# Kernel tuning notes

Hardware: AMD Instinct MI355X
Metric: run time of the kernel (lower is better)

Reference implementation:

```python
import jax, jax.numpy as jnp
import numpy as np

EPS = 1e-5  # torch GroupNorm default


def setup_inputs() -> dict:
    key = jax.random.key(0)
    k1, k2, k3 = jax.random.split(key, 3)
    bs, l, dim = 16, 2048, 512
    G, varDim, numCodes = 2, 256, 320
    x = jax.random.normal(k1, (bs, l, dim), dtype=jnp.float32)
    # grouped 1x1 Conv1d weight: (groups, out_per_group, in_per_group)
    proj_w = jax.random.normal(k2, (G, varDim, varDim), dtype=jnp.float32) / np.sqrt(varDim)
    gn_weight = jnp.ones((dim,), dtype=jnp.float32)
    gn_bias = jnp.zeros((dim,), dtype=jnp.float32)
    embeddings = 0.01 * jax.random.normal(k3, (numCodes, 1, varDim), dtype=jnp.float32)
    return {"x": x, "proj_w": proj_w, "gn_weight": gn_weight,
            "gn_bias": gn_bias, "embeddings": embeddings}


def reference(x, proj_w, gn_weight, gn_bias, embeddings):
    bs, l, dim = x.shape
    G, varDim, _ = proj_w.shape
    numCodes = embeddings.shape[0]

    # --- projection: grouped 1x1 conv ---
    xg = x.transpose(0, 2, 1).reshape(bs, G, varDim, l)            # (bs,G,v,l)
    ze_g = jnp.einsum('gov,bgvl->bgol', proj_w, xg)                # (bs,G,v,l)

    # --- Fp32GroupNorm over (C/G * L) per group ---
    zf = ze_g.astype(jnp.float32)
    mean = zf.mean(axis=(2, 3), keepdims=True)
    var = zf.var(axis=(2, 3), keepdims=True)
    zn = (zf - mean) * jax.lax.rsqrt(var + EPS)
    ze = zn.reshape(bs, dim, l) * gn_weight[None, :, None] + gn_bias[None, :, None]
    ze = ze.astype(x.dtype)                                        # (bs,dim,l)

    # --- VQ: nearest code per group (argmin of L2 == argmin of sq dist) ---
    z = ze.reshape(bs, G, varDim, l).transpose(0, 3, 1, 2)         # (bs,l,G,v)
    emb = jnp.broadcast_to(embeddings, (numCodes, G, varDim))      # combineGroups expand
    dots = jnp.einsum('blgv,cgv->blgc', z, emb)                    # (bs,l,G,C)
    e2 = jnp.sum(emb * emb, axis=-1)                               # (C,G)
    dist = e2.T[None, None] - 2.0 * dots                           # ||z||^2 dropped: const over C
    idx = jnp.argmin(dist, axis=-1)                                # (bs,l,G)

    # gather codes per group
    zq = jnp.take_along_axis(
        emb.transpose(1, 0, 2)[None, None],                        # (1,1,G,C,v)
        idx[..., None, None], axis=3).squeeze(3)                   # (bs,l,G,v)
    zq = zq.reshape(bs, l, dim)

    # straight-through estimator; output shape (bs, l, dim)
    ze_bld = ze.transpose(0, 2, 1)
    out = jax.lax.stop_gradient(zq) + ze_bld - jax.lax.stop_gradient(ze_bld)
    return out
```

## Files before the change

kernel.cpp:

```cpp
#include <hip/hip_runtime.h>
#include <math.h>

typedef _Float16 half8_t  __attribute__((ext_vector_type(8)));
typedef _Float16 half4_t  __attribute__((ext_vector_type(4)));
typedef float    floatx16 __attribute__((ext_vector_type(16)));

#define BS   16
#define LL   2048
#define DIMC 512
#define NG   2
#define VD   256
#define NC   320
#define NELEM ((double)(VD*LL))

#define GLL(gsrc, ldst) __builtin_amdgcn_global_load_lds( \
    (const __attribute__((address_space(1))) unsigned int*)(gsrc), \
    (__attribute__((address_space(3))) unsigned int*)(ldst), 16, 0, 0)

__global__ void k_prep(const float* __restrict__ W, const float* __restrict__ emb,
                       _Float16* __restrict__ Wimg, _Float16* __restrict__ Eimg,
                       float* __restrict__ e2f)
{
  const int blk = blockIdx.x, t = threadIdx.x;
  if (blk < 64) {
    int base = (blk * 256 + t) * 8;
    int k = base & 255, c = k >> 5, kk = k & 31;
    int row = (base >> 8) & 255, g = base >> 16;
    float4 v0 = *(const float4*)(W + base);
    float4 v1 = *(const float4*)(W + base + 4);
    float vv[8] = {v0.x, v0.y, v0.z, v0.w, v1.x, v1.y, v1.z, v1.w};
    half8_t hh, ll;
    #pragma unroll
    for (int i = 0; i < 8; ++i) {
      float s = vv[i] * 16.0f;
      _Float16 h = (_Float16)s;
      hh[i] = h; ll[i] = (_Float16)(s - (float)h);
    }
    size_t rb = ((size_t)(g * 8 + c) * 256 + row) * 72;
    *(half8_t*)&Wimg[rb + kk]      = hh;
    *(half8_t*)&Wimg[rb + 32 + kk] = ll;
  } else if (blk < 104) {
    int base = ((blk - 64) * 256 + t) * 8;
    int k = base & 255, c = k >> 5, kk = k & 31;
    int code = base >> 8;
    float4 v0 = *(const float4*)(emb + base);
    float4 v1 = *(const float4*)(emb + base + 4);
    float vv[8] = {v0.x, v0.y, v0.z, v0.w, v1.x, v1.y, v1.z, v1.w};
    half8_t hh, ll;
    #pragma unroll
    for (int i = 0; i < 8; ++i) {
      float s = vv[i] * 64.0f;
      _Float16 h = (_Float16)s;
      hh[i] = h; ll[i] = (_Float16)(s - (float)h);
    }
    size_t rb = ((size_t)c * 320 + code) * 72;
    *(half8_t*)&Eimg[rb + kk]      = hh;
    *(half8_t*)&Eimg[rb + 32 + kk] = ll;
  } else {
    int code = (blk - 104) * 256 + t;
    if (code < NC) {
      const float* er = emb + (size_t)code * VD;
      double s[4] = {0.0, 0.0, 0.0, 0.0};
      for (int v = 0; v < VD; v += 16)
        #pragma unroll
        for (int u = 0; u < 4; ++u) {
          float4 e4 = *(const float4*)(er + v + u * 4);
          s[u] += (double)e4.x * e4.x + (double)e4.y * e4.y
                + (double)e4.z * e4.z + (double)e4.w * e4.w;
        }
      e2f[code] = (float)(64.0 * (s[0] + s[1] + s[2] + s[3]));
    }
  }
}

__global__ __launch_bounds__(256, 2) void k_proj(
    const float* __restrict__ x, const _Float16* __restrict__ Wimg,
    float* __restrict__ ze, double* __restrict__ stats)
{
  __shared__ _Float16 Ah[128][72];
  __shared__ _Float16 Bh[256 * 72];

  const int blk = blockIdx.x;
  const int g  = blk & 1;
  const int m0 = (blk >> 1) * 128;
  const int b  = m0 >> 11;
  const int t  = threadIdx.x;
  const int lane = t & 63, w = t >> 6;
  const int col  = lane & 31, hq = lane >> 5;
  const int mw = (w & 1) * 64, nw = (w >> 1) * 128;

  const char* wbase = (const char*)(Wimg + (size_t)g * 8 * 256 * 72);

  floatx16 acc[2][4];
  #pragma unroll
  for (int i = 0; i < 2; ++i)
    #pragma unroll
    for (int j = 0; j < 4; ++j)
      #pragma unroll
      for (int e = 0; e < 16; ++e) acc[i][j][e] = 0.f;

  for (int c = 0; c < 8; ++c) {
    #pragma unroll
    for (int i = 0; i < 4; ++i) {
      int idx = i * 256 + t;
      int row = idx >> 3, kq = idx & 7;
      float4 v = *(const float4*)(x + ((size_t)(m0 + row)) * DIMC + g * VD + c * 32 + kq * 4);
      half4_t hh, ll;
      { _Float16 h = (_Float16)v.x; hh[0] = h; ll[0] = (_Float16)(v.x - (float)h); }
      { _Float16 h = (_Float16)v.y; hh[1] = h; ll[1] = (_Float16)(v.y - (float)h); }
      { _Float16 h = (_Float16)v.z; hh[2] = h; ll[2] = (_Float16)(v.z - (float)h); }
      { _Float16 h = (_Float16)v.w; hh[3] = h; ll[3] = (_Float16)(v.w - (float)h); }
      *(half4_t*)&Ah[row][kq * 4]      = hh;
      *(half4_t*)&Ah[row][32 + kq * 4] = ll;
    }
    {
      const char* wc = wbase + (size_t)c * 256 * 144;
      #pragma unroll
      for (int i = 0; i < 9; ++i) {
        int off = (w * 9 + i) * 1024 + lane * 16;
        GLL(wc + off, (char*)Bh + off);
      }
    }
    __syncthreads();
    #pragma unroll
    for (int ks = 0; ks < 2; ++ks) {
      const int ko = ks * 16 + hq * 8;
      half8_t azh[2], azl[2], bwh[4], bwl[4];
      #pragma unroll
      for (int i = 0; i < 2; ++i) {
        azh[i] = *(const half8_t*)&Ah[mw + i * 32 + col][ko];
        azl[i] = *(const half8_t*)&Ah[mw + i * 32 + col][32 + ko];
      }
      #pragma unroll
      for (int j = 0; j < 4; ++j) {
        bwh[j] = *(const half8_t*)&Bh[(nw + j * 32 + col) * 72 + ko];
        bwl[j] = *(const half8_t*)&Bh[(nw + j * 32 + col) * 72 + 32 + ko];
      }
      #pragma unroll
      for (int mi = 0; mi < 2; ++mi)
        #pragma unroll
        for (int ni = 0; ni < 4; ++ni) {
          acc[mi][ni] = __builtin_amdgcn_mfma_f32_32x32x16_f16(azh[mi], bwh[ni], acc[mi][ni], 0, 0, 0);
          acc[mi][ni] = __builtin_amdgcn_mfma_f32_32x32x16_f16(azh[mi], bwl[ni], acc[mi][ni], 0, 0, 0);
          acc[mi][ni] = __builtin_amdgcn_mfma_f32_32x32x16_f16(azl[mi], bwh[ni], acc[mi][ni], 0, 0, 0);
        }
    }
    __syncthreads();
  }

  double s1 = 0.0, s2 = 0.0;
  #pragma unroll
  for (int mi = 0; mi < 2; ++mi)
    #pragma unroll
    for (int ni = 0; ni < 4; ++ni)
      #pragma unroll
      for (int r = 0; r < 16; ++r) {
        float vv = acc[mi][ni][r] * 0.0625f;
        double d = (double)vv; s1 += d; s2 += d * d;
        int ml = mw + mi * 32 + (r & 3) + 8 * (r >> 2) + 4 * hq;
        int nl = nw + ni * 32 + col;
        ze[((size_t)(m0 + ml)) * DIMC + g * VD + nl] = vv;
      }
  #pragma unroll
  for (int off = 32; off > 0; off >>= 1) {
    s1 += __shfl_down(s1, off);
    s2 += __shfl_down(s2, off);
  }
  if (lane == 0) {
    atomicAdd(&stats[(b * NG + g) * 2 + 0], s1);
    atomicAdd(&stats[(b * NG + g) * 2 + 1], s2);
  }
}

__global__ __launch_bounds__(256, 2) void k_vq(
    float* __restrict__ zio, const float* __restrict__ emb,
    const _Float16* __restrict__ Eimg,
    const float* __restrict__ gnw, const float* __restrict__ gnb,
    const double* __restrict__ stats, const float* __restrict__ e2f)
{
  __shared__ _Float16 Zs[128][72];
  __shared__ _Float16 Es[320 * 72];
  __shared__ float e2sh[NC];
  __shared__ int idxs[128];

  const int blk = blockIdx.x;
  const int g  = blk & 1;
  const int m0 = (blk >> 1) * 128;
  const int b  = m0 >> 11;
  const int t  = threadIdx.x;
  const int lane = t & 63, w = t >> 6;
  const int col  = lane & 31, hq = lane >> 5;

  const int si = b * NG + g;
  double ss1 = stats[2 * si], ss2 = stats[2 * si + 1];
  double mu = ss1 / NELEM, var = ss2 / NELEM - mu * mu;
  const float mean = (float)mu;
  const float rstd = (float)(1.0 / sqrt(var + 1e-5));

  for (int c = t; c < NC; c += 256) e2sh[c] = e2f[c];

  float* zbase = zio + (size_t)m0 * DIMC + g * VD;
  const float* gw = gnw + g * VD;
  const float* gb = gnb + g * VD;

  floatx16 acc[10];
  #pragma unroll
  for (int i = 0; i < 10; ++i)
    #pragma unroll
    for (int e = 0; e < 16; ++e) acc[i][e] = 0.f;

  for (int c = 0; c < 8; ++c) {
    #pragma unroll
    for (int i = 0; i < 4; ++i) {
      int idx = i * 256 + t;
      int row = idx >> 3, kq = idx & 7;
      float4 v  = *(const float4*)(zbase + (size_t)row * DIMC + c * 32 + kq * 4);
      float4 w4 = *(const float4*)(gw + c * 32 + kq * 4);
      float4 b4 = *(const float4*)(gb + c * 32 + kq * 4);
      float zn0 = (v.x - mean) * rstd * w4.x + b4.x;
      float zn1 = (v.y - mean) * rstd * w4.y + b4.y;
      float zn2 = (v.z - mean) * rstd * w4.z + b4.z;
      float zn3 = (v.w - mean) * rstd * w4.w + b4.w;
      half4_t hh, ll;
      { _Float16 h = (_Float16)zn0; hh[0] = h; ll[0] = (_Float16)(zn0 - (float)h); }
      { _Float16 h = (_Float16)zn1; hh[1] = h; ll[1] = (_Float16)(zn1 - (float)h); }
      { _Float16 h = (_Float16)zn2; hh[2] = h; ll[2] = (_Float16)(zn2 - (float)h); }
      { _Float16 h = (_Float16)zn3; hh[3] = h; ll[3] = (_Float16)(zn3 - (float)h); }
      *(half4_t*)&Zs[row][kq * 4]      = hh;
      *(half4_t*)&Zs[row][32 + kq * 4] = ll;
    }
    {
      const char* ec = (const char*)Eimg + (size_t)c * 320 * 144;
      for (int i = w; i < 45; i += 4) {
        int off = i * 1024 + lane * 16;
        GLL(ec + off, (char*)Es + off);
      }
    }
    __syncthreads();
    #pragma unroll
    for (int ks = 0; ks < 2; ++ks) {
      const int ko = ks * 16 + hq * 8;
      half8_t bzh = *(const half8_t*)&Zs[w * 32 + col][ko];
      half8_t bzl = *(const half8_t*)&Zs[w * 32 + col][32 + ko];
      #pragma unroll
      for (int mt = 0; mt < 10; ++mt) {
        half8_t aeh = *(const half8_t*)&Es[(mt * 32 + col) * 72 + ko];
        half8_t ael = *(const half8_t*)&Es[(mt * 32 + col) * 72 + 32 + ko];
        acc[mt] = __builtin_amdgcn_mfma_f32_32x32x16_f16(aeh, bzh, acc[mt], 0, 0, 0);
        acc[mt] = __builtin_amdgcn_mfma_f32_32x32x16_f16(aeh, bzl, acc[mt], 0, 0, 0);
        acc[mt] = __builtin_amdgcn_mfma_f32_32x32x16_f16(ael, bzh, acc[mt], 0, 0, 0);
      }
    }
    __syncthreads();
  }

  float bv = 3.4e38f; int bi = 0x7fffffff;
  #pragma unroll
  for (int mt = 0; mt < 10; ++mt)
    #pragma unroll
    for (int r = 0; r < 16; ++r) {
      int code = mt * 32 + (r & 3) + 8 * (r >> 2) + 4 * hq;
      float d = e2sh[code] - 2.0f * acc[mt][r];
      if (d < bv || (d == bv && code < bi)) { bv = d; bi = code; }
    }
  {
    float ov = __shfl_xor(bv, 32);
    int   oi = __shfl_xor(bi, 32);
    if (ov < bv || (ov == bv && oi < bi)) { bv = ov; bi = oi; }
  }
  if (hq == 0) idxs[w * 32 + col] = bi;
  __syncthreads();

  #pragma unroll
  for (int it = 0; it < 32; ++it) {
    int idx = it * 256 + t;
    int row = idx >> 6, q4 = (idx & 63) * 4;
    int id = idxs[row];
    float4 e4 = *(const float4*)(emb + (size_t)id * VD + q4);
    *(float4*)(zbase + (size_t)row * DIMC + q4) = e4;
  }
}

extern "C" void kernel_launch(void* const* d_in, const int* in_sizes, int n_in,
                              void* d_out, int out_size, void* d_ws, size_t ws_size,
                              hipStream_t stream) {
  const float* x   = (const float*)d_in[0];
  const float* W   = (const float*)d_in[1];
  const float* gnw = (const float*)d_in[2];
  const float* gnb = (const float*)d_in[3];
  const float* emb = (const float*)d_in[4];
  float* out = (float*)d_out;

  double*   stats = (double*)d_ws;
  float*    e2f   = (float*)((char*)d_ws + 512);
  _Float16* Wimg  = (_Float16*)((char*)d_ws + 2048);
  _Float16* Eimg  = (_Float16*)((char*)d_ws + 591872);

  hipMemsetAsync(d_ws, 0, 512, stream);
  k_prep<<<106, 256, 0, stream>>>(W, emb, Wimg, Eimg, e2f);
  k_proj<<<512, 256, 0, stream>>>(x, Wimg, out, stats);
  k_vq<<<512, 256, 0, stream>>>(out, emb, Eimg, gnw, gnb, stats, e2f);
}
```

Before: 201.7 us.

## Fold prep kernel into projection kernel and replace stats atomics with per-block partials

Removes the separate k_prep launch and the memset. Each projection block now converts its W chunk from fp32 into split fp16 hi/lo form directly into LDS, and extra blocks appended to the grid build the embedding image and the code norms. The double atomics on the GroupNorm stats are replaced by per-block partial sums that k_vq adds up, which also removes the need to zero the stats buffer. The trade-off is that every projection block now repeats the W conversion with plain loads instead of async global_load_lds copies, adding redundant ALU and load work to cut launch and memset overhead.

```diff
diff --git a/kernel.cpp b/kernel.cpp
--- a/kernel.cpp
+++ b/kernel.cpp
@@ -17,30 +17,21 @@
     (const __attribute__((address_space(1))) unsigned int*)(gsrc), \
     (__attribute__((address_space(3))) unsigned int*)(ldst), 16, 0, 0)
 
-__global__ void k_prep(const float* __restrict__ W, const float* __restrict__ emb,
-                       _Float16* __restrict__ Wimg, _Float16* __restrict__ Eimg,
-                       float* __restrict__ e2f)
+__global__ __launch_bounds__(256, 2) void k_proj(
+    const float* __restrict__ x, const float* __restrict__ W,
+    const float* __restrict__ emb,
+    float* __restrict__ ze, double* __restrict__ pstats,
+    _Float16* __restrict__ Eimg, float* __restrict__ e2f)
 {
-  const int blk = blockIdx.x, t = threadIdx.x;
-  if (blk < 64) {
-    int base = (blk * 256 + t) * 8;
-    int k = base & 255, c = k >> 5, kk = k & 31;
-    int row = (base >> 8) & 255, g = base >> 16;
-    float4 v0 = *(const float4*)(W + base);
-    float4 v1 = *(const float4*)(W + base + 4);
-    float vv[8] = {v0.x, v0.y, v0.z, v0.w, v1.x, v1.y, v1.z, v1.w};
-    half8_t hh, ll;
-    #pragma unroll
-    for (int i = 0; i < 8; ++i) {
-      float s = vv[i] * 16.0f;
-      _Float16 h = (_Float16)s;
-      hh[i] = h; ll[i] = (_Float16)(s - (float)h);
-    }
-    size_t rb = ((size_t)(g * 8 + c) * 256 + row) * 72;
-    *(half8_t*)&Wimg[rb + kk]      = hh;
-    *(half8_t*)&Wimg[rb + 32 + kk] = ll;
-  } else if (blk < 104) {
-    int base = ((blk - 64) * 256 + t) * 8;
+  __shared__ _Float16 Ah[128][72];
+  __shared__ _Float16 Bh[256 * 72];
+  __shared__ double red[8];
+
+  const int blk = blockIdx.x;
+  const int t  = threadIdx.x;
+
+  if (blk >= 512) {
+    int base = ((blk - 512) * 256 + t) * 8;
     int k = base & 255, c = k >> 5, kk = k & 31;
     int code = base >> 8;
     float4 v0 = *(const float4*)(emb + base);
@@ -56,40 +47,29 @@
     size_t rb = ((size_t)c * 320 + code) * 72;
     *(half8_t*)&Eimg[rb + kk]      = hh;
     *(half8_t*)&Eimg[rb + 32 + kk] = ll;
-  } else {
-    int code = (blk - 104) * 256 + t;
-    if (code < NC) {
-      const float* er = emb + (size_t)code * VD;
-      double s[4] = {0.0, 0.0, 0.0, 0.0};
-      for (int v = 0; v < VD; v += 16)
-        #pragma unroll
-        for (int u = 0; u < 4; ++u) {
-          float4 e4 = *(const float4*)(er + v + u * 4);
-          s[u] += (double)e4.x * e4.x + (double)e4.y * e4.y
-                + (double)e4.z * e4.z + (double)e4.w * e4.w;
-        }
-      e2f[code] = (float)(64.0 * (s[0] + s[1] + s[2] + s[3]));
-    }
-  }
-}
-
-__global__ __launch_bounds__(256, 2) void k_proj(
-    const float* __restrict__ x, const _Float16* __restrict__ Wimg,
-    float* __restrict__ ze, double* __restrict__ stats)
-{
-  __shared__ _Float16 Ah[128][72];
-  __shared__ _Float16 Bh[256 * 72];
-
-  const int blk = blockIdx.x;
+    if (blk < 514) {
+      int cd = (blk - 512) * 256 + t;
+      if (cd < NC) {
+        const float* er = emb + (size_t)cd * VD;
+        double s[4] = {0.0, 0.0, 0.0, 0.0};
+        for (int v = 0; v < VD; v += 16)
+          #pragma unroll
+          for (int u = 0; u < 4; ++u) {
+            float4 e4 = *(const float4*)(er + v + u * 4);
+            s[u] += (double)e4.x * e4.x + (double)e4.y * e4.y
+                  + (double)e4.z * e4.z + (double)e4.w * e4.w;
+          }
+        e2f[cd] = (float)(64.0 * (s[0] + s[1] + s[2] + s[3]));
+      }
+    }
+    return;
+  }
+
   const int g  = blk & 1;
   const int m0 = (blk >> 1) * 128;
-  const int b  = m0 >> 11;
-  const int t  = threadIdx.x;
   const int lane = t & 63, w = t >> 6;
   const int col  = lane & 31, hq = lane >> 5;
   const int mw = (w & 1) * 64, nw = (w >> 1) * 128;
-
-  const char* wbase = (const char*)(Wimg + (size_t)g * 8 * 256 * 72);
 
   floatx16 acc[2][4];
   #pragma unroll
@@ -113,13 +93,23 @@
       *(half4_t*)&Ah[row][kq * 4]      = hh;
       *(half4_t*)&Ah[row][32 + kq * 4] = ll;
     }
-    {
-      const char* wc = wbase + (size_t)c * 256 * 144;
-      #pragma unroll
-      for (int i = 0; i < 9; ++i) {
-        int off = (w * 9 + i) * 1024 + lane * 16;
-        GLL(wc + off, (char*)Bh + off);
-      }
+    #pragma unroll
+    for (int i = 0; i < 4; ++i) {
+      int idx = i * 256 + t;
+      int row = idx >> 2, q = idx & 3;
+      const float* wp = W + ((size_t)(g * VD + row)) * VD + c * 32 + q * 8;
+      float4 v0 = *(const float4*)(wp);
+      float4 v1 = *(const float4*)(wp + 4);
+      float vv[8] = {v0.x, v0.y, v0.z, v0.w, v1.x, v1.y, v1.z, v1.w};
+      half8_t hh, ll;
+      #pragma unroll
+      for (int u = 0; u < 8; ++u) {
+        float s = vv[u] * 16.0f;
+        _Float16 h = (_Float16)s;
+        hh[u] = h; ll[u] = (_Float16)(s - (float)h);
+      }
+      *(half8_t*)&Bh[row * 72 + q * 8]      = hh;
+      *(half8_t*)&Bh[row * 72 + 32 + q * 8] = ll;
     }
     __syncthreads();
     #pragma unroll
@@ -166,9 +156,11 @@
     s1 += __shfl_down(s1, off);
     s2 += __shfl_down(s2, off);
   }
-  if (lane == 0) {
-    atomicAdd(&stats[(b * NG + g) * 2 + 0], s1);
-    atomicAdd(&stats[(b * NG + g) * 2 + 1], s2);
+  if (lane == 0) { red[w * 2] = s1; red[w * 2 + 1] = s2; }
+  __syncthreads();
+  if (t == 0) {
+    pstats[blk * 2 + 0] = red[0] + red[2] + red[4] + red[6];
+    pstats[blk * 2 + 1] = red[1] + red[3] + red[5] + red[7];
   }
 }
 
@@ -176,7 +168,7 @@
     float* __restrict__ zio, const float* __restrict__ emb,
     const _Float16* __restrict__ Eimg,
     const float* __restrict__ gnw, const float* __restrict__ gnb,
-    const double* __restrict__ stats, const float* __restrict__ e2f)
+    const double* __restrict__ pstats, const float* __restrict__ e2f)
 {
   __shared__ _Float16 Zs[128][72];
   __shared__ _Float16 Es[320 * 72];
@@ -191,8 +183,12 @@
   const int lane = t & 63, w = t >> 6;
   const int col  = lane & 31, hq = lane >> 5;
 
-  const int si = b * NG + g;
-  double ss1 = stats[2 * si], ss2 = stats[2 * si + 1];
+  double ss1 = 0.0, ss2 = 0.0;
+  #pragma unroll 4
+  for (int j = 0; j < 16; ++j) {
+    int pb = (((b * 16 + j) << 1) | g) * 2;
+    ss1 += pstats[pb]; ss2 += pstats[pb + 1];
+  }
   double mu = ss1 / NELEM, var = ss2 / NELEM - mu * mu;
   const float mean = (float)mu;
   const float rstd = (float)(1.0 / sqrt(var + 1e-5));
@@ -291,13 +287,10 @@
   const float* emb = (const float*)d_in[4];
   float* out = (float*)d_out;
 
-  double*   stats = (double*)d_ws;
-  float*    e2f   = (float*)((char*)d_ws + 512);
-  _Float16* Wimg  = (_Float16*)((char*)d_ws + 2048);
-  _Float16* Eimg  = (_Float16*)((char*)d_ws + 591872);
-
-  hipMemsetAsync(d_ws, 0, 512, stream);
-  k_prep<<<106, 256, 0, stream>>>(W, emb, Wimg, Eimg, e2f);
-  k_proj<<<512, 256, 0, stream>>>(x, Wimg, out, stats);
-  k_vq<<<512, 256, 0, stream>>>(out, emb, Eimg, gnw, gnb, stats, e2f);
+  double*   pstats = (double*)d_ws;
+  float*    e2f    = (float*)((char*)d_ws + 8192);
+  _Float16* Eimg   = (_Float16*)((char*)d_ws + 16384);
+
+  k_proj<<<552, 256, 0, stream>>>(x, W, emb, out, pstats, Eimg, e2f);
+  k_vq<<<512, 256, 0, stream>>>(out, emb, Eimg, gnw, gnb, pstats, e2f);
 }
```

Result: no change. 203.3 us (+0.8%).
